# Kernel optimization log

Hardware: AMD Instinct MI355X
Metric: run time of the kernel (lower is better)

## Reference

```python
import jax, jax.numpy as jnp
import numpy as np

HEADS = 16
D_MODEL = 1024
D_HEAD = D_MODEL // HEADS


def setup_inputs() -> dict:
    key = jax.random.key(0)
    ks = jax.random.split(key, 9)
    s_h = 1.0 / np.sqrt(D_HEAD)
    s_m = 1.0 / np.sqrt(D_MODEL)
    return {
        "x": jax.random.normal(ks[0], (4, 2048, D_MODEL), dtype=jnp.float32),
        "Wq": jax.random.uniform(ks[1], (D_HEAD, D_HEAD), jnp.float32, -s_h, s_h),
        "bq": jax.random.uniform(ks[2], (D_HEAD,), jnp.float32, -s_h, s_h),
        "Wk": jax.random.uniform(ks[3], (D_HEAD, D_HEAD), jnp.float32, -s_h, s_h),
        "bk": jax.random.uniform(ks[4], (D_HEAD,), jnp.float32, -s_h, s_h),
        "Wv": jax.random.uniform(ks[5], (D_HEAD, D_HEAD), jnp.float32, -s_h, s_h),
        "bv": jax.random.uniform(ks[6], (D_HEAD,), jnp.float32, -s_h, s_h),
        "Wp": jax.random.uniform(ks[7], (D_MODEL, D_MODEL), jnp.float32, -s_m, s_m),
        "bp": jax.random.uniform(ks[8], (D_MODEL,), jnp.float32, -s_m, s_m),
    }


def reference(x, Wq, bq, Wk, bk, Wv, bv, Wp, bp):
    B, T, C = x.shape
    xh = x.reshape(B, T, HEADS, D_HEAD)  # [B,T,H,Dh]
    # per-head linear projections (torch Linear: x @ W.T + b)
    q = jnp.einsum('bthd,ed->bhte', xh, Wq) + bq  # [B,H,T,Dh]
    k = jnp.einsum('bthd,ed->bhte', xh, Wk) + bk
    v = jnp.einsum('bthd,ed->bhte', xh, Wv) + bv
    # NOTE: original scales by sqrt(C) = sqrt(d_model), not sqrt(d_head)
    att = jnp.einsum('bhqd,bhkd->bhqk', q, k) / jnp.sqrt(jnp.float32(C))
    att = jax.nn.softmax(att, axis=-1)
    out = jnp.einsum('bhqk,bhkd->bhqd', att, v)  # [B,H,T,Dh]
    out = out.transpose(0, 2, 1, 3).reshape(B, T, C)
    return out @ Wp.T + bp
```

## Files before the change

### kernel.cpp

```cpp
#include <hip/hip_runtime.h>
#include <hip/hip_bf16.h>
#include <cstddef>

#define B_  4
#define T_  2048
#define H_  16
#define DH  64
#define C_  1024
#define BH  64

typedef float  f32x16 __attribute__((ext_vector_type(16)));
typedef __bf16 bf16x8 __attribute__((ext_vector_type(8)));
typedef unsigned int u32;
typedef const __attribute__((address_space(1))) u32* gas_u32p;
typedef __attribute__((address_space(3))) u32* las_u32p;

#define MFMA32(a, b, c) __builtin_amdgcn_mfma_f32_32x32x16_bf16(a, b, c, 0, 0, 0)


__device__ __forceinline__ unsigned pack2(float a, float b) {
    return ((unsigned)__builtin_bit_cast(unsigned short, (__bf16)b) << 16)
         | (unsigned)__builtin_bit_cast(unsigned short, (__bf16)a);
}

__device__ __forceinline__ void dma8(const __bf16* gbase, size_t rowstride,
                                     __bf16* lds_rowbase, int r8, int lane)
{
    const int r = r8 + (lane >> 3);
    const int j = (lane & 7) ^ (r & 7);
    const __bf16* src = gbase + (size_t)r * rowstride + j * 8;
    __builtin_amdgcn_global_load_lds((gas_u32p)src, (las_u32p)lds_rowbase,
                                     16, 0, 0);
}

__device__ __forceinline__ bf16x8 frag(const __bf16* tile, int row, int chunk)
{
    return *(const bf16x8*)&tile[row * 64 + (((chunk ^ (row & 7))) << 3)];
}

__global__ __launch_bounds__(256) void qkv_kernel(
    const float* __restrict__ x,
    const float* __restrict__ Wq, const float* __restrict__ bq,
    const float* __restrict__ Wk, const float* __restrict__ bk,
    const float* __restrict__ Wv, const float* __restrict__ bv,
    const float* __restrict__ Wp, __bf16* __restrict__ Wp16,
    __bf16* __restrict__ q, __bf16* __restrict__ k, __bf16* __restrict__ vt)
{
    __shared__ __bf16 Xs[128 * 72];
    __shared__ __bf16 Ws[3][64 * 72];
    __bf16* Vtl = Xs;

    const int tt  = blockIdx.x;
    const int bh  = blockIdx.y;
    const int b   = bh >> 4, h = bh & 15;
    const int t0  = tt * 128;
    const int tid = threadIdx.x;
    const int wave = tid >> 6, lane = tid & 63;
    const int m = lane & 31, hh = lane >> 5;

    {
        const int flat = (bh * 16 + tt) * 256 + tid;
        const float4 w4 = *(const float4*)(Wp + (size_t)flat * 4);
        uint2 pk; pk.x = pack2(w4.x, w4.y); pk.y = pack2(w4.z, w4.w);
        *(uint2*)(Wp16 + (size_t)flat * 4) = pk;
    }

    #pragma unroll
    for (int i = 0; i < 8; ++i) {
        const int idx = i * 256 + tid;
        const int r = idx >> 4, c = (idx & 15) * 4;
        const float4 x4 = *(const float4*)(x + ((size_t)(b * T_ + t0 + r)) * C_ + h * DH + c);
        *(unsigned*)&Xs[r * 72 + c]     = pack2(x4.x, x4.y);
        *(unsigned*)&Xs[r * 72 + c + 2] = pack2(x4.z, x4.w);
    }
    #pragma unroll
    for (int i = 0; i < 4; ++i) {
        const int idx = i * 256 + tid;
        const int r = idx >> 4, c = (idx & 15) * 4;
        const float* wsrc[3] = {Wq, Wk, Wv};
        #pragma unroll
        for (int wv_ = 0; wv_ < 3; ++wv_) {
            const float4 w4 = *(const float4*)(wsrc[wv_] + r * 64 + c);
            *(unsigned*)&Ws[wv_][r * 72 + c]     = pack2(w4.x, w4.y);
            *(unsigned*)&Ws[wv_][r * 72 + c + 2] = pack2(w4.z, w4.w);
        }
    }
    __syncthreads();

    bf16x8 xf[4];
    #pragma unroll
    for (int ks = 0; ks < 4; ++ks)
        xf[ks] = *(const bf16x8*)&Xs[(wave * 32 + m) * 72 + ks * 16 + hh * 8];
    __syncthreads();

    const float sQ = 0.03125f * 1.44269504f;

    #pragma unroll
    for (int mat = 0; mat < 3; ++mat) {
        f32x16 acc0 = {}, acc1 = {};
        #pragma unroll
        for (int ks = 0; ks < 4; ++ks) {
            const bf16x8 w0 = *(const bf16x8*)&Ws[mat][(m) * 72 + ks * 16 + hh * 8];
            const bf16x8 w1 = *(const bf16x8*)&Ws[mat][(32 + m) * 72 + ks * 16 + hh * 8];
            acc0 = MFMA32(xf[ks], w0, acc0);
            acc1 = MFMA32(xf[ks], w1, acc1);
        }
        const float* bias = (mat == 0) ? bq : (mat == 1) ? bk : bv;
        const float b0 = bias[m], b1 = bias[32 + m];
        #pragma unroll
        for (int r = 0; r < 16; ++r) {
            const int R = (r & 3) + 8 * (r >> 2) + 4 * hh;
            const int tloc = wave * 32 + R;
            const float v0 = acc0[r] + b0, v1 = acc1[r] + b1;
            if (mat == 0) {
                const size_t base = ((size_t)bh * T_ + t0 + tloc) * DH;
                q[base + m]      = (__bf16)(v0 * sQ);
                q[base + 32 + m] = (__bf16)(v1 * sQ);
            } else if (mat == 1) {
                const size_t base = ((size_t)bh * T_ + t0 + tloc) * DH;
                k[base + m]      = (__bf16)v0;
                k[base + 32 + m] = (__bf16)v1;
            } else {
                Vtl[(m) * 136 + tloc]      = (__bf16)v0;
                Vtl[(32 + m) * 136 + tloc] = (__bf16)v1;
            }
        }
    }
    __syncthreads();
    #pragma unroll
    for (int i = 0; i < 4; ++i) {
        const int idx = i * 256 + tid;
        const int e = idx >> 4, c = (idx & 15) * 8;
        *(uint4*)(vt + ((size_t)(bh * 64 + e)) * T_ + t0 + c) = *(uint4*)&Vtl[e * 136 + c];
    }
}

__global__ __launch_bounds__(256, 3) void attn_kernel(
    const __bf16* __restrict__ q, const __bf16* __restrict__ k,
    const __bf16* __restrict__ vt, __bf16* __restrict__ o)
{
    __shared__ __bf16 PQs[128 * 72];
    __shared__ __bf16 Ks[2][64 * 64];
    __shared__ __bf16 Vts[2][64 * 64];

    const int bh  = blockIdx.y;
    const int q0  = blockIdx.x * 128;
    const int tid = threadIdx.x;
    const int wave = tid >> 6, lane = tid & 63;
    const int m = lane & 31, h = lane >> 5;
    const int qrow0 = wave * 32;

    const __bf16* qb = q  + (size_t)bh * T_ * DH;
    const __bf16* kb = k  + (size_t)bh * T_ * DH;
    const __bf16* vb = vt + (size_t)bh * DH * T_;

    #pragma unroll
    for (int s = 0; s < 2; ++s) {
        const int r8 = wave * 16 + s * 8;
        dma8(kb, DH, &Ks[0][r8 * 64], r8, lane);
        dma8(vb, T_, &Vts[0][r8 * 64], r8, lane);
    }
    #pragma unroll
    for (int i = 0; i < 4; ++i) {
        const int idx = i * 256 + tid;
        const int r = idx >> 3, c = (idx & 7) * 8;
        *(uint4*)&PQs[r * 72 + c] = *(const uint4*)(qb + (size_t)(q0 + r) * DH + c);
    }
    __syncthreads();

    bf16x8 qf[4];
    #pragma unroll
    for (int ks = 0; ks < 4; ++ks)
        qf[ks] = *(const bf16x8*)&PQs[(qrow0 + m) * 72 + ks * 16 + h * 8];

    f32x16 O0 = {}, O1 = {};
    float lsum[16];
    #pragma unroll
    for (int r = 0; r < 16; ++r) lsum[r] = 0.f;

    #pragma unroll 2
    for (int it = 0; it < 32; ++it) {
        const int cur = it & 1;

        if (it < 31) {
            #pragma unroll
            for (int s = 0; s < 2; ++s) {
                const int r8 = wave * 16 + s * 8;
                dma8(kb + (size_t)(it + 1) * 64 * DH, DH, &Ks[cur ^ 1][r8 * 64], r8, lane);
                dma8(vb + (it + 1) * 64,              T_, &Vts[cur ^ 1][r8 * 64], r8, lane);
            }
        }

        f32x16 S0 = {}, S1 = {};
        #pragma unroll
        for (int ks = 0; ks < 4; ++ks) {
            const bf16x8 k0 = frag(Ks[cur], m,      ks * 2 + h);
            const bf16x8 k1 = frag(Ks[cur], 32 + m, ks * 2 + h);
            S0 = MFMA32(qf[ks], k0, S0);
            S1 = MFMA32(qf[ks], k1, S1);
        }

        #pragma unroll
        for (int r = 0; r < 16; ++r) {
            const int R = (r & 3) + 8 * (r >> 2) + 4 * h;
            const float p0 = exp2f(S0[r]);
            const float p1 = exp2f(S1[r]);
            lsum[r] += p0 + p1;
            PQs[(qrow0 + R) * 72 + m]      = (__bf16)p0;
            PQs[(qrow0 + R) * 72 + 32 + m] = (__bf16)p1;
        }

        #pragma unroll
        for (int ks = 0; ks < 4; ++ks) {
            const bf16x8 pf = *(const bf16x8*)&PQs[(qrow0 + m) * 72 + ks * 16 + h * 8];
            const bf16x8 v0 = frag(Vts[cur], m,      ks * 2 + h);
            const bf16x8 v1 = frag(Vts[cur], 32 + m, ks * 2 + h);
            O0 = MFMA32(pf, v0, O0);
            O1 = MFMA32(pf, v1, O1);
        }

        __syncthreads();
    }

    #pragma unroll
    for (int r = 0; r < 16; ++r) {
        float s = lsum[r];
        s += __shfl_xor(s, 1);  s += __shfl_xor(s, 2);  s += __shfl_xor(s, 4);
        s += __shfl_xor(s, 8);  s += __shfl_xor(s, 16);
        lsum[r] = 1.0f / s;
    }
    __bf16* ob = o + (size_t)bh * T_ * DH;
    #pragma unroll
    for (int r = 0; r < 16; ++r) {
        const int R = (r & 3) + 8 * (r >> 2) + 4 * h;
        const size_t row = (size_t)(q0 + qrow0 + R) * DH;
        ob[row + m]      = (__bf16)(O0[r] * lsum[r]);
        ob[row + 32 + m] = (__bf16)(O1[r] * lsum[r]);
    }
}

__global__ __launch_bounds__(256, 2) void proj_kernel(
    const __bf16* __restrict__ a,
    const __bf16* __restrict__ Wp16, const float* __restrict__ bp,
    float* __restrict__ out)
{
    __shared__ __bf16 As[2][128 * 64];
    __shared__ __bf16 Bs[2][128 * 64];

    const int tb = blockIdx.x, eb = blockIdx.y;
    const int tid = threadIdx.x;
    const int wave = tid >> 6, lane = tid & 63;
    const int m = lane & 31, h = lane >> 5;
    const int tok0 = tb * 128;
    const int b = tok0 >> 11, t0 = tok0 & (T_ - 1);
    const int e0 = eb * 128;

    #pragma unroll
    for (int s = 0; s < 4; ++s) {
        const int r8 = wave * 32 + s * 8;
        dma8(a + ((size_t)(b * H_) * T_ + t0) * DH, DH, &As[0][r8 * 64], r8, lane);
        dma8(Wp16 + (size_t)e0 * C_, C_, &Bs[0][r8 * 64], r8, lane);
    }
    __syncthreads();

    f32x16 acc[4] = {f32x16{}, f32x16{}, f32x16{}, f32x16{}};

    #pragma unroll 2
    for (int cb = 0; cb < 16; ++cb) {
        const int cur = cb & 1;
        if (cb < 15) {
            #pragma unroll
            for (int s = 0; s < 4; ++s) {
                const int r8 = wave * 32 + s * 8;
                dma8(a + ((size_t)(b * H_ + cb + 1) * T_ + t0) * DH, DH,
                     &As[cur ^ 1][r8 * 64], r8, lane);
                dma8(Wp16 + (size_t)e0 * C_ + (cb + 1) * 64, C_,
                     &Bs[cur ^ 1][r8 * 64], r8, lane);
            }
        }

        #pragma unroll
        for (int ks = 0; ks < 4; ++ks) {
            const bf16x8 af = frag(As[cur], wave * 32 + m, ks * 2 + h);
            #pragma unroll
            for (int n = 0; n < 4; ++n) {
                const bf16x8 bf = frag(Bs[cur], n * 32 + m, ks * 2 + h);
                acc[n] = MFMA32(af, bf, acc[n]);
            }
        }
        __syncthreads();
    }

    #pragma unroll
    for (int n = 0; n < 4; ++n) {
        const int e = e0 + n * 32 + m;
        const float bias = bp[e];
        #pragma unroll
        for (int r = 0; r < 16; ++r) {
            const int R = (r & 3) + 8 * (r >> 2) + 4 * h;
            out[(size_t)(tok0 + wave * 32 + R) * C_ + e] = acc[n][r] + bias;
        }
    }
}

extern "C" void kernel_launch(void* const* d_in, const int* in_sizes, int n_in,
                              void* d_out, int out_size, void* d_ws, size_t ws_size,
                              hipStream_t stream)
{
    const float* x  = (const float*)d_in[0];
    const float* Wq = (const float*)d_in[1];
    const float* bq = (const float*)d_in[2];
    const float* Wk = (const float*)d_in[3];
    const float* bk = (const float*)d_in[4];
    const float* Wv = (const float*)d_in[5];
    const float* bv = (const float*)d_in[6];
    const float* Wp = (const float*)d_in[7];
    const float* bp = (const float*)d_in[8];

    const size_t N = (size_t)BH * T_ * DH;
    __bf16* qws  = (__bf16*)d_ws;
    __bf16* kws  = qws + N;
    __bf16* vtws = kws + N;
    __bf16* ows  = vtws + N;
    __bf16* wp16 = ows + N;

    qkv_kernel<<<dim3(16, 64), 256, 0, stream>>>(
        x, Wq, bq, Wk, bk, Wv, bv, Wp, wp16, qws, kws, vtws);
    attn_kernel<<<dim3(16, 64), 256, 0, stream>>>(qws, kws, vtws, ows);
    proj_kernel<<<dim3(64, 8), 256, 0, stream>>>(ows, wp16, bp, (float*)d_out);
}
```

Before: 251.8 us.

## Compute transposed scores to keep P in registers, drop async double buffering

```diff
diff --git a/kernel.cpp b/kernel.cpp
--- a/kernel.cpp
+++ b/kernel.cpp
@@ -32,7 +32,6 @@
     __builtin_amdgcn_global_load_lds((gas_u32p)src, (las_u32p)lds_rowbase,
                                      16, 0, 0);
 }
-
 __device__ __forceinline__ bf16x8 frag(const __bf16* tile, int row, int chunk)
 {
     return *(const bf16x8*)&tile[row * 64 + (((chunk ^ (row & 7))) << 3)];
@@ -139,9 +138,9 @@
     const __bf16* __restrict__ q, const __bf16* __restrict__ k,
     const __bf16* __restrict__ vt, __bf16* __restrict__ o)
 {
-    __shared__ __bf16 PQs[128 * 72];
-    __shared__ __bf16 Ks[2][64 * 64];
-    __shared__ __bf16 Vts[2][64 * 64];
+    __shared__ __bf16 Ks[64 * 72];
+    __shared__ __bf16 Vts[64 * 72];
+    __shared__ float  Ls[128];
 
     const int bh  = blockIdx.y;
     const int q0  = blockIdx.x * 128;
@@ -154,88 +153,76 @@
     const __bf16* kb = k  + (size_t)bh * T_ * DH;
     const __bf16* vb = vt + (size_t)bh * DH * T_;
 
-    #pragma unroll
-    for (int s = 0; s < 2; ++s) {
-        const int r8 = wave * 16 + s * 8;
-        dma8(kb, DH, &Ks[0][r8 * 64], r8, lane);
-        dma8(vb, T_, &Vts[0][r8 * 64], r8, lane);
-    }
-    #pragma unroll
-    for (int i = 0; i < 4; ++i) {
-        const int idx = i * 256 + tid;
-        const int r = idx >> 3, c = (idx & 7) * 8;
-        *(uint4*)&PQs[r * 72 + c] = *(const uint4*)(qb + (size_t)(q0 + r) * DH + c);
-    }
-    __syncthreads();
-
     bf16x8 qf[4];
     #pragma unroll
     for (int ks = 0; ks < 4; ++ks)
-        qf[ks] = *(const bf16x8*)&PQs[(qrow0 + m) * 72 + ks * 16 + h * 8];
+        qf[ks] = *(const bf16x8*)(qb + (size_t)(q0 + qrow0 + m) * DH + ks * 16 + h * 8);
 
     f32x16 O0 = {}, O1 = {};
-    float lsum[16];
-    #pragma unroll
-    for (int r = 0; r < 16; ++r) lsum[r] = 0.f;
-
-    #pragma unroll 2
-    for (int it = 0; it < 32; ++it) {
-        const int cur = it & 1;
-
-        if (it < 31) {
-            #pragma unroll
-            for (int s = 0; s < 2; ++s) {
-                const int r8 = wave * 16 + s * 8;
-                dma8(kb + (size_t)(it + 1) * 64 * DH, DH, &Ks[cur ^ 1][r8 * 64], r8, lane);
-                dma8(vb + (it + 1) * 64,              T_, &Vts[cur ^ 1][r8 * 64], r8, lane);
-            }
-        }
-
-        f32x16 S0 = {}, S1 = {};
+    float lsum = 0.f;
+
+    for (int kt = 0; kt < T_; kt += 64) {
+        __syncthreads();
+        #pragma unroll
+        for (int i = 0; i < 2; ++i) {
+            const int idx = i * 256 + tid;
+            const int r = idx >> 3, c = (idx & 7) * 8;
+            *(uint4*)&Ks[r * 72 + c]  = *(const uint4*)(kb + (size_t)(kt + r) * DH + c);
+            *(uint4*)&Vts[r * 72 + c] = *(const uint4*)(vb + (size_t)r * T_ + kt + c);
+        }
+        __syncthreads();
+
+        f32x16 St0 = {}, St1 = {};
         #pragma unroll
         for (int ks = 0; ks < 4; ++ks) {
-            const bf16x8 k0 = frag(Ks[cur], m,      ks * 2 + h);
-            const bf16x8 k1 = frag(Ks[cur], 32 + m, ks * 2 + h);
-            S0 = MFMA32(qf[ks], k0, S0);
-            S1 = MFMA32(qf[ks], k1, S1);
-        }
-
-        #pragma unroll
-        for (int r = 0; r < 16; ++r) {
-            const int R = (r & 3) + 8 * (r >> 2) + 4 * h;
-            const float p0 = exp2f(S0[r]);
-            const float p1 = exp2f(S1[r]);
-            lsum[r] += p0 + p1;
-            PQs[(qrow0 + R) * 72 + m]      = (__bf16)p0;
-            PQs[(qrow0 + R) * 72 + 32 + m] = (__bf16)p1;
+            const bf16x8 k0 = *(const bf16x8*)&Ks[(m) * 72 + ks * 16 + h * 8];
+            const bf16x8 k1 = *(const bf16x8*)&Ks[(32 + m) * 72 + ks * 16 + h * 8];
+            St0 = MFMA32(k0, qf[ks], St0);
+            St1 = MFMA32(k1, qf[ks], St1);
+        }
+
+        u32 pk0[8], pk1[8];
+        #pragma unroll
+        for (int i = 0; i < 8; ++i) {
+            const float a0 = exp2f(St0[2 * i]), a1 = exp2f(St0[2 * i + 1]);
+            const float b0 = exp2f(St1[2 * i]), b1 = exp2f(St1[2 * i + 1]);
+            lsum += a0 + a1 + b0 + b1;
+            pk0[i] = pack2(a0, a1);
+            pk1[i] = pack2(b0, b1);
         }
 
         #pragma unroll
         for (int ks = 0; ks < 4; ++ks) {
-            const bf16x8 pf = *(const bf16x8*)&PQs[(qrow0 + m) * 72 + ks * 16 + h * 8];
-            const bf16x8 v0 = frag(Vts[cur], m,      ks * 2 + h);
-            const bf16x8 v1 = frag(Vts[cur], 32 + m, ks * 2 + h);
+            const u32* pk = (ks < 2) ? pk0 : pk1;
+            const int G4 = (ks & 1) * 4;
+            const u32 s0 = h ? pk[G4]     : pk[G4 + 2];
+            const u32 s1 = h ? pk[G4 + 1] : pk[G4 + 3];
+            const u32 r0 = (u32)__shfl_xor((int)s0, 32);
+            const u32 r1 = (u32)__shfl_xor((int)s1, 32);
+            uint4 w;
+            w.x = h ? r0         : pk[G4];
+            w.y = h ? r1         : pk[G4 + 1];
+            w.z = h ? pk[G4 + 2] : r0;
+            w.w = h ? pk[G4 + 3] : r1;
+            const bf16x8 pf = __builtin_bit_cast(bf16x8, w);
+            const bf16x8 v0 = *(const bf16x8*)&Vts[(m) * 72 + ks * 16 + h * 8];
+            const bf16x8 v1 = *(const bf16x8*)&Vts[(32 + m) * 72 + ks * 16 + h * 8];
             O0 = MFMA32(pf, v0, O0);
             O1 = MFMA32(pf, v1, O1);
         }
-
-        __syncthreads();
-    }
-
-    #pragma unroll
-    for (int r = 0; r < 16; ++r) {
-        float s = lsum[r];
-        s += __shfl_xor(s, 1);  s += __shfl_xor(s, 2);  s += __shfl_xor(s, 4);
-        s += __shfl_xor(s, 8);  s += __shfl_xor(s, 16);
-        lsum[r] = 1.0f / s;
-    }
+    }
+
+    const float tot = lsum + __shfl_xor(lsum, 32);
+    if (h == 0) Ls[qrow0 + m] = 1.0f / tot;
+
     __bf16* ob = o + (size_t)bh * T_ * DH;
     #pragma unroll
     for (int r = 0; r < 16; ++r) {
         const int R = (r & 3) + 8 * (r >> 2) + 4 * h;
+        const float inv = Ls[qrow0 + R];
         const size_t row = (size_t)(q0 + qrow0 + R) * DH;
-        ob[row + m]      = (__bf16)(O0[r] * lsum[r]);
-        ob[row + 32 + m] = (__bf16)(O1[r] * lsum[r]);
+        ob[row + m]      = (__bf16)(O0[r] * inv);
+        ob[row + 32 + m] = (__bf16)(O1[r] * inv);
     }
 }
 
```

After: 256.5 us. No clear change (+1.9%).
